# Kernel tuning notes

Measured on AMD Instinct MI355X. Metric: run time of the kernel, lower is better.

## Reference

```python
import math
import jax, jax.numpy as jnp
import numpy as np

D = 256       # d_model
R = 64        # low-rank bottleneck
E = 3         # num experts
KS = (1, 3, 5)
EPS = 0.1     # sinkhorn epsilon
ITERS = 10    # sinkhorn iterations


def _ln(x, g, b):
    m = jnp.mean(x, -1, keepdims=True)
    v = jnp.mean((x - m) ** 2, -1, keepdims=True)
    return (x - m) * jax.lax.rsqrt(v + 1e-5) * g + b


def _gelu(x):
    return jax.nn.gelu(x, approximate=False)  # torch nn.GELU default (erf)


def setup_inputs() -> dict:
    key = jax.random.key(0)
    ks = jax.random.split(key, 12)
    s = 0.02
    B, Lt, La = 16, 1024, 2048
    return {
        "text_feat": jax.random.normal(ks[0], (B, Lt, D), jnp.float32),
        "audio_feat": jax.random.normal(ks[1], (B, La, D), jnp.float32),
        # shared OT projection (LayerNorm + Linear, shared across modalities)
        "ln_g": jnp.ones((D,), jnp.float32),
        "ln_b": jnp.zeros((D,), jnp.float32),
        "W_sh": jax.random.normal(ks[2], (D, D), jnp.float32) * s,
        "b_sh": jnp.zeros((D,), jnp.float32),
        # contradiction router: Linear(d+1->d) GELU Linear(d->E)
        "Wr1": jax.random.normal(ks[3], (D, D + 1), jnp.float32) * s,
        "br1": jnp.zeros((D,), jnp.float32),
        "Wr2": jax.random.normal(ks[4], (E, D), jnp.float32) * s,
        "br2": jnp.zeros((E,), jnp.float32),
        # 3 low-rank conv experts (stacked where shapes match)
        "down_W": jax.random.normal(ks[5], (E, R, D), jnp.float32) * s,
        "down_b": jnp.zeros((E, R), jnp.float32),
        "conv_w1": jax.random.normal(ks[6], (R, R, 1), jnp.float32) * s,
        "conv_w3": jax.random.normal(ks[7], (R, R, 3), jnp.float32) * s,
        "conv_w5": jax.random.normal(ks[8], (R, R, 5), jnp.float32) * s,
        "conv_b": jnp.zeros((E, R), jnp.float32),
        "up_W": jax.random.normal(ks[9], (E, D, R), jnp.float32) * s,
        "up_b": jnp.zeros((E, D), jnp.float32),
        "en_g": jnp.ones((E, D), jnp.float32),
        "en_b": jnp.zeros((E, D), jnp.float32),
    }


def reference(text_feat, audio_feat, ln_g, ln_b, W_sh, b_sh, Wr1, br1, Wr2, br2,
              down_W, down_b, conv_w1, conv_w3, conv_w5, conv_b, up_W, up_b, en_g, en_b):
    B, Lt, _ = text_feat.shape
    La = audio_feat.shape[1]

    # ---- shared projection (dropout = identity at eval) ----
    Tp = _ln(text_feat, ln_g, ln_b) @ W_sh.T + b_sh      # [B,Lt,D]
    Ap = _ln(audio_feat, ln_g, ln_b) @ W_sh.T + b_sh     # [B,La,D]

    # ---- cosine cost ----
    Tn = Tp / jnp.maximum(jnp.linalg.norm(Tp, axis=-1, keepdims=True), 1e-12)
    An = Ap / jnp.maximum(jnp.linalg.norm(Ap, axis=-1, keepdims=True), 1e-12)
    cost = 1.0 - jnp.einsum('bmd,bnd->bmn', Tn, An)      # [B,Lt,La]

    # ---- log-domain Sinkhorn (uniform marginals, no masks) ----
    log_K = -cost / (EPS + 1e-8)
    log_mu = jnp.full((B, Lt), -math.log(Lt), jnp.float32)
    log_nu = jnp.full((B, La), -math.log(La), jnp.float32)
    lu = jnp.zeros((B, Lt), jnp.float32)
    lv = jnp.zeros((B, La), jnp.float32)
    for _ in range(ITERS):
        lu = log_mu - jax.scipy.special.logsumexp(log_K + lv[:, None, :], axis=-1)
        lu = jnp.nan_to_num(jnp.clip(lu, -1e9, 1e9), nan=0.0, posinf=1e9, neginf=-1e9)
        lv = log_nu - jax.scipy.special.logsumexp(log_K + lu[:, :, None], axis=1)
        lv = jnp.nan_to_num(jnp.clip(lv, -1e9, 1e9), nan=0.0, posinf=1e9, neginf=-1e9)
    pi = jnp.exp(lu[:, :, None] + log_K + lv[:, None, :])
    pi = jnp.nan_to_num(pi, nan=0.0, posinf=1.0, neginf=0.0)  # [B,Lt,La]

    A_al = jnp.einsum('bmn,bnd->bmd', pi, Ap)            # [B,Lt,D]
    S = jnp.sum(Tp * A_al, -1)                           # [B,Lt]
    resid = jnp.abs(Tp - A_al)                           # [B,Lt,D]

    # ---- contradiction router ----
    rin = jnp.concatenate([S[..., None], resid], -1)     # [B,Lt,D+1]
    G = jax.nn.softmax(_gelu(rin @ Wr1.T + br1) @ Wr2.T + br2, axis=-1)  # [B,Lt,E]

    # ---- multi-scale low-rank conv MoE over contradiction residual ----
    convs = (conv_w1, conv_w3, conv_w5)
    x = resid
    out = jnp.zeros_like(Tp)
    for e in range(E):
        h = _gelu(x @ down_W[e].T + down_b[e])           # [B,Lt,R]
        k = convs[e].shape[-1]
        pad = (k - 1) // 2
        hc = jax.lax.conv_general_dilated(
            h.transpose(0, 2, 1), convs[e], (1,), [(pad, pad)],
            dimension_numbers=('NCH', 'OIH', 'NCH')) + conv_b[e][None, :, None]
        h = _gelu(hc).transpose(0, 2, 1)                 # [B,Lt,R]
        h = h @ up_W[e].T + up_b[e]                      # [B,Lt,D]
        eo = _ln(h + x, en_g[e], en_b[e])
        out = out + G[..., e:e + 1] * eo
    return out
```

## Files before the change

### kernel.cpp

```cpp
#include <hip/hip_runtime.h>
#include <cstdio>

#define D_ 256
#define LT 1024
#define LA 2048
#define NB 16
#define RR_ 64
#define NRT (NB*LT)
#define NRA (NB*LA)

#define DECQ  (-0.080645161f)
#define DECQ2 (-0.11634637f)

typedef short bf16x8 __attribute__((ext_vector_type(8)));
typedef float f32x4 __attribute__((ext_vector_type(4)));

__device__ __forceinline__ float gelu_f(float x) {
    return 0.5f * x * (1.0f + erff(x * 0.70710678118654752f));
}
__device__ __forceinline__ unsigned short f2bf(float f) {
    union { float f; unsigned int i; } c; c.f = f;
    unsigned int x = c.i;
    return (unsigned short)((x + 0x7fffu + ((x >> 16) & 1u)) >> 16);
}
__device__ __forceinline__ float exp2_fast(float x) {
#if __has_builtin(__builtin_amdgcn_exp2f)
    return __builtin_amdgcn_exp2f(x);
#else
    float r; asm("v_exp_f32 %0, %1" : "=v"(r) : "v"(x)); return r;
#endif
}
__device__ __forceinline__ unsigned int cvt_pk_bf16(float lo, float hi) {
    unsigned int r;
    asm("v_cvt_pk_bf16_f32 %0, %1, %2" : "=v"(r) : "v"(lo), "v"(hi));
    return r;
}

__global__ __launch_bounds__(256) void k_prep_all(
    const float* __restrict__ W_sh, const float* __restrict__ down_W,
    const float* __restrict__ up_W, const float* __restrict__ Wr1,
    unsigned short* __restrict__ Wb, unsigned short* __restrict__ dWb,
    unsigned short* __restrict__ uWb, unsigned short* __restrict__ Wr1b)
{
    int i = blockIdx.x * 256 + threadIdx.x;
    if (i < 65536) Wb[i] = f2bf(W_sh[i]);
    else if (i < 114688) { int j = i - 65536; dWb[j] = f2bf(down_W[j]); }
    else if (i < 163840) { int j = i - 114688; uWb[j] = f2bf(up_W[j]); }
    else { int j = i - 163840; int n = j >> 8, k = j & 255; Wr1b[j] = f2bf(Wr1[(long)n * 257 + 1 + k]); }
}

__global__ __launch_bounds__(256) void k_lnproj_fused(
    const float* __restrict__ Xt, const float* __restrict__ Xa,
    const float* __restrict__ g, const float* __restrict__ bln,
    const unsigned short* __restrict__ Wb, const float* __restrict__ bsh,
    float* __restrict__ Tp, unsigned short* __restrict__ Tnb,
    unsigned short* __restrict__ Anb, unsigned short* __restrict__ ApbT)
{
    __shared__ short smem[64 * 264 + 256 * 40];
    short (*xb)[264] = (short(*)[264])smem;
    short (*Bs)[40]  = (short(*)[40])(smem + 64 * 264);
    short (*tt)[72]  = (short(*)[72])smem;
    int tid = threadIdx.x;
    int bid = blockIdx.x;
    bool is_text = bid < (NRT / 64);
    const float* X = is_text ? Xt : Xa;
    long row0 = is_text ? (long)bid * 64 : (long)(bid - NRT / 64) * 64;
    {
        int lane = tid & 31, rg = tid >> 5;
        float4 ga = *(const float4*)(g + lane * 8);
        float4 gb2 = *(const float4*)(g + lane * 8 + 4);
        float4 ba = *(const float4*)(bln + lane * 8);
        float4 bb2 = *(const float4*)(bln + lane * 8 + 4);
        for (int it = 0; it < 8; it++) {
            int r = it * 8 + rg;
            const float4* xp4 = (const float4*)(X + (row0 + r) * D_);
            float4 a = xp4[lane * 2], b = xp4[lane * 2 + 1];
            float s = a.x + a.y + a.z + a.w + b.x + b.y + b.z + b.w;
#pragma unroll
            for (int off = 16; off >= 1; off >>= 1) s += __shfl_xor(s, off);
            float mean = s * (1.0f / 256.0f);
            float q = (a.x - mean) * (a.x - mean) + (a.y - mean) * (a.y - mean)
                    + (a.z - mean) * (a.z - mean) + (a.w - mean) * (a.w - mean)
                    + (b.x - mean) * (b.x - mean) + (b.y - mean) * (b.y - mean)
                    + (b.z - mean) * (b.z - mean) + (b.w - mean) * (b.w - mean);
#pragma unroll
            for (int off = 16; off >= 1; off >>= 1) q += __shfl_xor(q, off);
            float ivar = rsqrtf(q * (1.0f / 256.0f) + 1e-5f);
            float v0 = (a.x - mean) * ivar * ga.x + ba.x;
            float v1 = (a.y - mean) * ivar * ga.y + ba.y;
            float v2 = (a.z - mean) * ivar * ga.z + ba.z;
            float v3 = (a.w - mean) * ivar * ga.w + ba.w;
            float v4 = (b.x - mean) * ivar * gb2.x + bb2.x;
            float v5 = (b.y - mean) * ivar * gb2.y + bb2.y;
            float v6 = (b.z - mean) * ivar * gb2.z + bb2.z;
            float v7 = (b.w - mean) * ivar * gb2.w + bb2.w;
            int4 pv;
            pv.x = (int)cvt_pk_bf16(v0, v1); pv.y = (int)cvt_pk_bf16(v2, v3);
            pv.z = (int)cvt_pk_bf16(v4, v5); pv.w = (int)cvt_pk_bf16(v6, v7);
            *(int4*)&xb[r][lane * 8] = pv;
        }
    }
    __syncthreads();
    int wid = tid >> 6, lane = tid & 63;
    int l15 = lane & 15, kq = lane >> 4;
    int m_local = wid * 16;
    f32x4 acc[16];
#pragma unroll
    for (int j = 0; j < 16; j++) acc[j] = (f32x4){0.f, 0.f, 0.f, 0.f};
    for (int kt = 0; kt < 8; kt++) {
        int k0 = kt * 32;
#pragma unroll
        for (int h = 0; h < 4; h++) {
            int idx = tid + 256 * h;
            int n = idx >> 2, qc = idx & 3;
            *(int4*)&Bs[n][qc * 8] = *(const int4*)(Wb + (long)n * D_ + k0 + qc * 8);
        }
        __syncthreads();
        bf16x8 af = *(const bf16x8*)&xb[m_local + l15][k0 + kq * 8];
#pragma unroll
        for (int j = 0; j < 16; j++) {
            bf16x8 bf = *(const bf16x8*)&Bs[j * 16 + l15][kq * 8];
            acc[j] = __builtin_amdgcn_mfma_f32_16x16x32_bf16(af, bf, acc[j], 0, 0, 0);
        }
        __syncthreads();
    }
#pragma unroll
    for (int j = 0; j < 16; j++) {
        float bv = bsh[j * 16 + l15];
#pragma unroll
        for (int r = 0; r < 4; r++) acc[j][r] += bv;
    }
    float sq[4] = {0.f, 0.f, 0.f, 0.f};
#pragma unroll
    for (int j = 0; j < 16; j++)
#pragma unroll
        for (int r = 0; r < 4; r++) sq[r] += acc[j][r] * acc[j][r];
#pragma unroll
    for (int off = 8; off >= 1; off >>= 1) {
#pragma unroll
        for (int r = 0; r < 4; r++) sq[r] += __shfl_xor(sq[r], off);
    }
    float rinv[4];
#pragma unroll
    for (int r = 0; r < 4; r++) rinv[r] = 1.0f / fmaxf(sqrtf(sq[r]), 1e-12f);
    if (is_text) {
#pragma unroll
        for (int j = 0; j < 16; j++) {
            int col = j * 16 + l15;
#pragma unroll
            for (int r = 0; r < 4; r++) {
                long m = row0 + m_local + kq * 4 + r;
                Tp[m * D_ + col] = acc[j][r];
                Tnb[m * D_ + col] = f2bf(acc[j][r] * rinv[r]);
            }
        }
    } else {
#pragma unroll
        for (int j = 0; j < 16; j++) {
            int col = j * 16 + l15;
#pragma unroll
            for (int r = 0; r < 4; r++) {
                int rloc = m_local + kq * 4 + r;
                unsigned short qv = f2bf(acc[j][r] * rinv[r]);
                Anb[(row0 + rloc) * D_ + col] = qv;
                tt[col][rloc] = (short)qv;
            }
        }
        __syncthreads();
        int b = (int)(row0 >> 11);
        int n0 = (int)(row0 & 2047);
#pragma unroll
        for (int h = 0; h < 8; h++) {
            int ci = tid + 256 * h;
            int col = ci >> 3, nch = ci & 7;
            int4 v = *(const int4*)&tt[col][nch * 8];
            *(int4*)(ApbT + ((long)b * D_ + col) * LA + n0 + nch * 8) = v;
        }
    }
}

__global__ __launch_bounds__(256) void k_cost_mfma(
    const unsigned short* __restrict__ Tnb, const unsigned short* __restrict__ Anb,
    unsigned char* __restrict__ logK8, unsigned char* __restrict__ logK8T)
{
    __shared__ short sm[2][128][48];
    short (*As)[48] = sm[0];
    short (*Bs)[48] = sm[1];
    unsigned char* tile = (unsigned char*)sm;
    int b = blockIdx.x;
    int m_blk = blockIdx.y * 128, n_blk = blockIdx.z * 128;
    int tid = threadIdx.x;
    int wid = tid >> 6, lane = tid & 63;
    int l15 = lane & 15, kq = lane >> 4;
    int wm0 = (wid >> 1) * 64, wn0 = (wid & 1) * 64;
    const unsigned short* Ab = Tnb + ((long)b * LT + m_blk) * D_;
    const unsigned short* Bb = Anb + ((long)b * LA + n_blk) * D_;
    f32x4 acc[4][4];
#pragma unroll
    for (int i = 0; i < 4; i++)
#pragma unroll
        for (int j = 0; j < 4; j++) acc[i][j] = (f32x4){0.f, 0.f, 0.f, 0.f};
    for (int kt = 0; kt < 8; kt++) {
        int k0 = kt * 32;
#pragma unroll
        for (int h = 0; h < 2; h++) {
            int idx = tid + 256 * h;
            int row = idx >> 2, ch = idx & 3;
            *(int4*)&As[row][ch * 8] = *(const int4*)(Ab + (long)row * D_ + k0 + ch * 8);
            *(int4*)&Bs[row][ch * 8] = *(const int4*)(Bb + (long)row * D_ + k0 + ch * 8);
        }
        __syncthreads();
        bf16x8 af[4], bfv[4];
#pragma unroll
        for (int i = 0; i < 4; i++) af[i] = *(const bf16x8*)&As[wm0 + i * 16 + l15][kq * 8];
#pragma unroll
        for (int j = 0; j < 4; j++) bfv[j] = *(const bf16x8*)&Bs[wn0 + j * 16 + l15][kq * 8];
#pragma unroll
        for (int i = 0; i < 4; i++)
#pragma unroll
            for (int j = 0; j < 4; j++)
                acc[i][j] = __builtin_amdgcn_mfma_f32_16x16x32_bf16(af[i], bfv[j], acc[i][j], 0, 0, 0);
        __syncthreads();
    }
#pragma unroll
    for (int i = 0; i < 4; i++) {
#pragma unroll
        for (int j = 0; j < 4; j++) {
            int n = wn0 + j * 16 + l15;
            long base = ((long)b * LT + m_blk + wm0 + i * 16 + kq * 4) * (long)LA + n_blk + n;
            unsigned int pk = 0;
#pragma unroll
            for (int r = 0; r < 4; r++) {
                float q = rintf((1.0f - acc[i][j][r]) * 124.0f);
                q = fminf(fmaxf(q, 0.0f), 255.0f);
                unsigned int qb = (unsigned int)q;
                pk |= qb << (8 * r);
                logK8[base + (long)r * LA] = (unsigned char)qb;
            }
            *(unsigned int*)&tile[n * 144 + wm0 + i * 16 + kq * 4] = pk;
        }
    }
    __syncthreads();
#pragma unroll
    for (int h = 0; h < 4; h++) {
        int idx = tid + 256 * h;
        int row = idx >> 3, ch = idx & 7;
        int4 v = *(const int4*)&tile[row * 144 + ch * 16];
        *(int4*)(logK8T + ((long)b * LA + n_blk + row) * (long)LT + m_blk + ch * 16) = v;
    }
}

__global__ __launch_bounds__(256) void k_rowlse3(
    const unsigned char* __restrict__ logK8, const float* __restrict__ lv2,
    float* __restrict__ lu2, int first)
{
    __shared__ float red[2][2];
    int b = blockIdx.x & 15;
    int mseg = blockIdx.x >> 4;
    int tid = threadIdx.x;
    int row = tid >> 7;
    int ln = tid & 127;
    float lvv[16];
    if (!first) {
        const float* lvp = lv2 + (long)b * LA + ln * 16;
#pragma unroll
        for (int k = 0; k < 4; k++) {
            float4 l = *(const float4*)(lvp + k * 4);
            lvv[k * 4 + 0] = l.x; lvv[k * 4 + 1] = l.y;
            lvv[k * 4 + 2] = l.z; lvv[k * 4 + 3] = l.w;
        }
    } else {
#pragma unroll
        for (int k = 0; k < 16; k++) lvv[k] = 0.f;
    }
    const unsigned char* p = logK8 + ((long)b * LT + mseg * 2 + row) * (long)LA + ln * 16;
    uint4 w = *(const uint4*)p;
    unsigned int ws4[4] = {w.x, w.y, w.z, w.w};
    float s = 0.f;
#pragma unroll
    for (int k = 0; k < 4; k++) {
        unsigned int u = ws4[k];
        s += exp2_fast(fmaf((float)(u & 0xffu),         DECQ2, lvv[k * 4 + 0]));
        s += exp2_fast(fmaf((float)((u >> 8) & 0xffu),  DECQ2, lvv[k * 4 + 1]));
        s += exp2_fast(fmaf((float)((u >> 16) & 0xffu), DECQ2, lvv[k * 4 + 2]));
        s += exp2_fast(fmaf((float)(u >> 24),           DECQ2, lvv[k * 4 + 3]));
    }
#pragma unroll
    for (int off = 32; off >= 1; off >>= 1) s += __shfl_xor(s, off);
    if ((tid & 63) == 0) red[row][(tid >> 6) & 1] = s;
    __syncthreads();
    if (tid < 2) {
        float sr = red[tid][0] + red[tid][1];
        lu2[(long)b * LT + mseg * 2 + tid] = -10.0f - __log2f(sr);
    }
}

__global__ __launch_bounds__(256) void k_collse3(
    const unsigned char* __restrict__ logK8T, const float* __restrict__ lu2,
    float* __restrict__ lv2)
{
    int b = blockIdx.x & 15;
    int nseg = blockIdx.x >> 4;
    int tid = threadIdx.x;
    int wv = tid >> 6, lane = tid & 63;
    int c = nseg * 4 + wv;
    float lus[16];
    const float* lup = lu2 + (long)b * LT + lane * 16;
#pragma unroll
    for (int k = 0; k < 4; k++) {
        float4 l = *(const float4*)(lup + k * 4);
        lus[k * 4 + 0] = l.x; lus[k * 4 + 1] = l.y;
        lus[k * 4 + 2] = l.z; lus[k * 4 + 3] = l.w;
    }
    const unsigned char* p = logK8T + ((long)b * LA + c) * (long)LT + lane * 16;
    uint4 w = *(const uint4*)p;
    unsigned int ws4[4] = {w.x, w.y, w.z, w.w};
    float s = 0.f;
#pragma unroll
    for (int k = 0; k < 4; k++) {
        unsigned int u = ws4[k];
        s += exp2_fast(fmaf((float)(u & 0xffu),         DECQ2, lus[k * 4 + 0]));
        s += exp2_fast(fmaf((float)((u >> 8) & 0xffu),  DECQ2, lus[k * 4 + 1]));
        s += exp2_fast(fmaf((float)((u >> 16) & 0xffu), DECQ2, lus[k * 4 + 2]));
        s += exp2_fast(fmaf((float)(u >> 24),           DECQ2, lus[k * 4 + 3]));
    }
#pragma unroll
    for (int off = 32; off >= 1; off >>= 1) s += __shfl_xor(s, off);
    if (lane == 0) lv2[(long)b * LA + c] = -11.0f - __log2f(s);
}

__global__ __launch_bounds__(256) void k_pi2(
    const unsigned char* __restrict__ logK8, const unsigned short* __restrict__ Ap,
    const float* __restrict__ lu2, const float* __restrict__ lv2,
    float* __restrict__ Apart)
{
    __shared__ short As[64][56];
    __shared__ short Bs[256][56];
    __shared__ float lv_s[1024];
    __shared__ float eus[64];
    int b = blockIdx.x;
    int kh = blockIdx.y;
    int m_blk = blockIdx.z * 64;
    int nbase = kh * 1024;
    int tid = threadIdx.x;
    for (int i = tid; i < 1024; i += 256) lv_s[i] = lv2[(long)b * LA + nbase + i];
    if (tid < 64) eus[tid] = exp2_fast(lu2[(long)b * LT + m_blk + tid]);
    __syncthreads();
    int wid = tid >> 6, lane = tid & 63;
    int l15 = lane & 15, kq = lane >> 4;
    int wm0 = (wid & 1) * 32, wd0 = (wid >> 1) * 128;
    f32x4 acc[2][8];
#pragma unroll
    for (int i = 0; i < 2; i++)
#pragma unroll
        for (int j = 0; j < 8; j++) acc[i][j] = (f32x4){0.f, 0.f, 0.f, 0.f};
    const unsigned char* Kbase = logK8 + ((long)b * LT + m_blk) * (long)LA + nbase;
    const unsigned short* Bbase = Ap + (long)b * D_ * (long)LA + nbase;
    int arow = tid >> 2, ac8 = (tid & 3) * 8;
    for (int kt = 0; kt < 32; kt++) {
        int n0 = kt * 32;
        {
            uint2 raw = *(const uint2*)(Kbase + (long)arow * LA + n0 + ac8);
            const float* lvp = &lv_s[n0 + ac8];
            unsigned int w0 = raw.x, w1 = raw.y;
            float e0 = exp2_fast(fmaf((float)(w0 & 0xffu),         DECQ2, lvp[0]));
            float e1 = exp2_fast(fmaf((float)((w0 >> 8) & 0xffu),  DECQ2, lvp[1]));
            float e2 = exp2_fast(fmaf((float)((w0 >> 16) & 0xffu), DECQ2, lvp[2]));
            float e3 = exp2_fast(fmaf((float)(w0 >> 24),           DECQ2, lvp[3]));
            float e4 = exp2_fast(fmaf((float)(w1 & 0xffu),         DECQ2, lvp[4]));
            float e5 = exp2_fast(fmaf((float)((w1 >> 8) & 0xffu),  DECQ2, lvp[5]));
            float e6 = exp2_fast(fmaf((float)((w1 >> 16) & 0xffu), DECQ2, lvp[6]));
            float e7 = exp2_fast(fmaf((float)(w1 >> 24),           DECQ2, lvp[7]));
            int4 ov;
            ov.x = (int)cvt_pk_bf16(e0, e1); ov.y = (int)cvt_pk_bf16(e2, e3);
            ov.z = (int)cvt_pk_bf16(e4, e5); ov.w = (int)cvt_pk_bf16(e6, e7);
            *(int4*)&As[arow][ac8] = ov;
        }
#pragma unroll
        for (int h = 0; h < 4; h++) {
            int idx = tid + 256 * h;
            int row = idx >> 2, ch = idx & 3;
            *(int4*)&Bs[row][ch * 8] = *(const int4*)(Bbase + (long)row * LA + n0 + ch * 8);
        }
        __syncthreads();
        bf16x8 af[2], bfv[8];
        af[0] = *(const bf16x8*)&As[wm0 + l15][kq * 8];
        af[1] = *(const bf16x8*)&As[wm0 + 16 + l15][kq * 8];
#pragma unroll
        for (int j = 0; j < 8; j++) bfv[j] = *(const bf16x8*)&Bs[wd0 + j * 16 + l15][kq * 8];
#pragma unroll
        for (int i = 0; i < 2; i++)
#pragma unroll
            for (int j = 0; j < 8; j++)
                acc[i][j] = __builtin_amdgcn_mfma_f32_16x16x32_bf16(af[i], bfv[j], acc[i][j], 0, 0, 0);
        __syncthreads();
    }
    float* dst = Apart + (long)kh * (NB * (long)LT * D_);
#pragma unroll
    for (int i = 0; i < 2; i++) {
#pragma unroll
        for (int r = 0; r < 4; r++) {
            int rloc = wm0 + i * 16 + kq * 4 + r;
            float eu = eus[rloc];
            int m = m_blk + rloc;
            long obase = ((long)b * LT + m) * D_;
#pragma unroll
            for (int j = 0; j < 8; j++)
                dst[obase + wd0 + j * 16 + l15] = acc[i][j][r] * eu;
        }
    }
}

__global__ __launch_bounds__(256) void k_sresid(
    const float* __restrict__ Tp, const float* __restrict__ Apart,
    float* __restrict__ resid, unsigned short* __restrict__ residb, float* __restrict__ S)
{
    __shared__ float red[4];
    int b = blockIdx.x & 15;
    int m = blockIdx.x >> 4;
    long row = (long)b * LT + m;
    int tid = threadIdx.x;
    long idx = row * D_ + tid;
    float t = Tp[idx];
    float a = Apart[idx] + Apart[idx + (long)NB * LT * D_];
    float rr = fabsf(t - a);
    resid[idx] = rr;
    residb[idx] = f2bf(rr);
    float p = t * a;
#pragma unroll
    for (int off = 32; off >= 1; off >>= 1) p += __shfl_xor(p, off);
    if ((tid & 63) == 0) red[tid >> 6] = p;
    __syncthreads();
    if (tid == 0) S[row] = red[0] + red[1] + red[2] + red[3];
}

__global__ __launch_bounds__(256) void k_router_fused(
    const unsigned short* __restrict__ residb, const unsigned short* __restrict__ Wr1b,
    const float* __restrict__ Wr1, const float* __restrict__ br1,
    const float* __restrict__ S, const float* __restrict__ Wr2,
    const float* __restrict__ br2, float* __restrict__ G)
{
    __shared__ short xb[16][264];
    __shared__ short Bs[256][40];
    __shared__ float red[4][3][16];
    int tid = threadIdx.x;
    long row0 = (long)blockIdx.x * 16;
#pragma unroll
    for (int h = 0; h < 2; h++) {
        int idx = tid + 256 * h;
        int row = idx >> 5, ch = idx & 31;
        *(int4*)&xb[row][ch * 8] = *(const int4*)(residb + (row0 + row) * D_ + ch * 8);
    }
    __syncthreads();
    int wid = tid >> 6, lane = tid & 63;
    int l15 = lane & 15, kq = lane >> 4;
    f32x4 acc[4];
#pragma unroll
    for (int j = 0; j < 4; j++) acc[j] = (f32x4){0.f, 0.f, 0.f, 0.f};
    for (int kt = 0; kt < 8; kt++) {
        int k0 = kt * 32;
#pragma unroll
        for (int h = 0; h < 4; h++) {
            int idx = tid + 256 * h;
            int n = idx >> 2, qc = idx & 3;
            *(int4*)&Bs[n][qc * 8] = *(const int4*)(Wr1b + (long)n * D_ + k0 + qc * 8);
        }
        __syncthreads();
        bf16x8 af = *(const bf16x8*)&xb[l15][k0 + kq * 8];
#pragma unroll
        for (int j = 0; j < 4; j++) {
            bf16x8 bf = *(const bf16x8*)&Bs[wid * 64 + j * 16 + l15][kq * 8];
            acc[j] = __builtin_amdgcn_mfma_f32_16x16x32_bf16(af, bf, acc[j], 0, 0, 0);
        }
        __syncthreads();
    }
    float sv[4];
#pragma unroll
    for (int r = 0; r < 4; r++) sv[r] = S[row0 + kq * 4 + r];
    float le[3][4] = {};
#pragma unroll
    for (int j = 0; j < 4; j++) {
        int col = wid * 64 + j * 16 + l15;
        float w0 = Wr1[(long)col * 257];
        float bv = br1[col];
        float w2a = Wr2[col], w2b = Wr2[256 + col], w2c = Wr2[512 + col];
#pragma unroll
        for (int r = 0; r < 4; r++) {
            float hv = gelu_f(acc[j][r] + sv[r] * w0 + bv);
            le[0][r] += hv * w2a;
            le[1][r] += hv * w2b;
            le[2][r] += hv * w2c;
        }
    }
#pragma unroll
    for (int off = 8; off >= 1; off >>= 1)
#pragma unroll
        for (int e = 0; e < 3; e++)
#pragma unroll
            for (int r = 0; r < 4; r++) le[e][r] += __shfl_xor(le[e][r], off);
    if (l15 == 0) {
#pragma unroll
        for (int e = 0; e < 3; e++)
#pragma unroll
            for (int r = 0; r < 4; r++) red[wid][e][kq * 4 + r] = le[e][r];
    }
    __syncthreads();
    if (tid < 16) {
        float L0 = red[0][0][tid] + red[1][0][tid] + red[2][0][tid] + red[3][0][tid] + br2[0];
        float L1 = red[0][1][tid] + red[1][1][tid] + red[2][1][tid] + red[3][1][tid] + br2[1];
        float L2 = red[0][2][tid] + red[1][2][tid] + red[2][2][tid] + red[3][2][tid] + br2[2];
        float mx = fmaxf(L0, fmaxf(L1, L2));
        float e0 = __expf(L0 - mx), e1 = __expf(L1 - mx), e2 = __expf(L2 - mx);
        float inv = 1.0f / (e0 + e1 + e2);
        long m = row0 + tid;
        G[m] = e0 * inv; G[NRT + m] = e1 * inv; G[2 * NRT + m] = e2 * inv;
    }
}

__global__ __launch_bounds__(256) void k_down_mfma(
    const unsigned short* __restrict__ residb, const unsigned short* __restrict__ dWb,
    const float* __restrict__ db, float* __restrict__ hall)
{
    __shared__ short xb[64][264];
    __shared__ short Bs[64][40];
    int tid = threadIdx.x;
    int e = blockIdx.y;
    int b = blockIdx.x & 15;
    int mseg = blockIdx.x >> 4;
    long row0 = (long)b * LT + mseg * 64;
    const unsigned short* dWe = dWb + (long)e * RR_ * D_;
    float* h = hall + (long)e * NRT * RR_;
#pragma unroll
    for (int hh = 0; hh < 8; hh++) {
        int idx = tid + 256 * hh;
        int row = idx >> 5, ch = idx & 31;
        *(int4*)&xb[row][ch * 8] = *(const int4*)(residb + (row0 + row) * D_ + ch * 8);
    }
    __syncthreads();
    int wid = tid >> 6, lane = tid & 63;
    int l15 = lane & 15, kq = lane >> 4;
    int m_local = wid * 16;
    f32x4 acc[4];
#pragma unroll
    for (int j = 0; j < 4; j++) acc[j] = (f32x4){0.f, 0.f, 0.f, 0.f};
    for (int kt = 0; kt < 8; kt++) {
        int k0 = kt * 32;
        {
            int n = tid >> 2, qc = tid & 3;
            *(int4*)&Bs[n][qc * 8] = *(const int4*)(dWe + (long)n * D_ + k0 + qc * 8);
        }
        __syncthreads();
        bf16x8 af = *(const bf16x8*)&xb[m_local + l15][k0 + kq * 8];
#pragma unroll
        for (int j = 0; j < 4; j++) {
            bf16x8 bf = *(const bf16x8*)&Bs[j * 16 + l15][kq * 8];
            acc[j] = __builtin_amdgcn_mfma_f32_16x16x32_bf16(af, bf, acc[j], 0, 0, 0);
        }
        __syncthreads();
    }
#pragma unroll
    for (int j = 0; j < 4; j++) {
        int col = j * 16 + l15;
        float bv = db[e * RR_ + col];
#pragma unroll
        for (int r = 0; r < 4; r++) {
            long m = row0 + m_local + kq * 4 + r;
            h[m * RR_ + col] = gelu_f(acc[j][r] + bv);
        }
    }
}

__global__ __launch_bounds__(256) void k_conv_all(
    const float* __restrict__ hall, const float* __restrict__ cw1,
    const float* __restrict__ cw3, const float* __restrict__ cw5,
    const float* __restrict__ conv_b, unsigned short* __restrict__ hcbb)
{
    __shared__ float hs[68][68];
    __shared__ float wt[64][64];
    int e = blockIdx.y;
    const float* w = (e == 0) ? cw1 : ((e == 1) ? cw3 : cw5);
    int ksz = (e == 0) ? 1 : ((e == 1) ? 3 : 5);
    const float* h = hall + (long)e * NRT * RR_;
    unsigned short* hcb = hcbb + (long)e * NRT * RR_;
    const float* cb = conv_b + e * 64;
    int b = blockIdx.x & 15;
    int m0 = (blockIdx.x >> 4) * 64;
    int tid = threadIdx.x;
    int pad = (ksz - 1) >> 1;
    for (int idx = tid; idx < 68 * 16; idx += 256) {
        int mr = idx >> 4, i4 = idx & 15;
        int mm = m0 - 2 + mr;
        float4 vv = { 0.f, 0.f, 0.f, 0.f };
        if (mm >= 0 && mm < LT) vv = *(const float4*)(h + ((long)b * LT + mm) * RR_ + i4 * 4);
        *(float4*)&hs[mr][i4 * 4] = vv;
    }
    int tx = tid & 15, ty = tid >> 4;
    float acc[4][4] = {};
    for (int t = 0; t < ksz; t++) {
        __syncthreads();
        for (int idx = tid; idx < 4096; idx += 256) {
            int i = idx & 63, j = idx >> 6;
            wt[i][j] = w[(long)j * RR_ * ksz + i * ksz + t];
        }
        __syncthreads();
        int roff = ty * 4 + 2 + t - pad;
        for (int i4 = 0; i4 < 16; i4++) {
            float4 h0 = *(const float4*)&hs[roff + 0][i4 * 4];
            float4 h1 = *(const float4*)&hs[roff + 1][i4 * 4];
            float4 h2 = *(const float4*)&hs[roff + 2][i4 * 4];
            float4 h3 = *(const float4*)&hs[roff + 3][i4 * 4];
            float hh[4][4] = { { h0.x, h0.y, h0.z, h0.w }, { h1.x, h1.y, h1.z, h1.w },
                               { h2.x, h2.y, h2.z, h2.w }, { h3.x, h3.y, h3.z, h3.w } };
#pragma unroll
            for (int s = 0; s < 4; s++) {
                float4 wv = *(const float4*)&wt[i4 * 4 + s][tx * 4];
#pragma unroll
                for (int r = 0; r < 4; r++) {
                    acc[r][0] += hh[r][s] * wv.x;
                    acc[r][1] += hh[r][s] * wv.y;
                    acc[r][2] += hh[r][s] * wv.z;
                    acc[r][3] += hh[r][s] * wv.w;
                }
            }
        }
    }
    float4 bb = *(const float4*)(cb + tx * 4);
#pragma unroll
    for (int r = 0; r < 4; r++) {
        long m = (long)b * LT + m0 + ty * 4 + r;
        unsigned long long pv =
              (unsigned long long)cvt_pk_bf16(gelu_f(acc[r][0] + bb.x), gelu_f(acc[r][1] + bb.y))
            | ((unsigned long long)cvt_pk_bf16(gelu_f(acc[r][2] + bb.z), gelu_f(acc[r][3] + bb.w)) << 32);
        *(unsigned long long*)(hcb + m * RR_ + tx * 4) = pv;
    }
}

__global__ __launch_bounds__(256) void k_up3(
    const unsigned short* __restrict__ hcbb, const unsigned short* __restrict__ uWb,
    const float* __restrict__ up_b, const float* __restrict__ resid,
    const float* __restrict__ en_g, const float* __restrict__ en_b,
    const float* __restrict__ G, float* __restrict__ out)
{
    __shared__ short hs[64][88];
    __shared__ short Bs[256][40];
    int tid = threadIdx.x;
    int b = blockIdx.x & 15;
    int mseg = blockIdx.x >> 4;
    long row0 = (long)b * LT + mseg * 64;
    int wid = tid >> 6, lane = tid & 63;
    int l15 = lane & 15, kq = lane >> 4;
    int m_local = wid * 16;
    long mrow[4];
#pragma unroll
    for (int r = 0; r < 4; r++) mrow[r] = row0 + m_local + kq * 4 + r;
    f32x4 outacc[16];
#pragma unroll
    for (int j = 0; j < 16; j++) outacc[j] = (f32x4){0.f, 0.f, 0.f, 0.f};
    for (int e = 0; e < 3; e++) {
        __syncthreads();
        const unsigned short* hcb = hcbb + (long)e * NRT * RR_;
        const unsigned short* uWe = uWb + (long)e * 16384;
#pragma unroll
        for (int hh = 0; hh < 2; hh++) {
            int idx = tid + 256 * hh;
            int row = idx >> 3, ch = idx & 7;
            *(int4*)&hs[row][ch * 8] = *(const int4*)(hcb + (row0 + row) * RR_ + ch * 8);
        }
        f32x4 acc[16];
#pragma unroll
        for (int j = 0; j < 16; j++) acc[j] = (f32x4){0.f, 0.f, 0.f, 0.f};
        for (int kt = 0; kt < 2; kt++) {
            int k0 = kt * 32;
#pragma unroll
            for (int hh = 0; hh < 4; hh++) {
                int idx = tid + 256 * hh;
                int n = idx >> 2, qc = idx & 3;
                *(int4*)&Bs[n][qc * 8] = *(const int4*)(uWe + (long)n * RR_ + k0 + qc * 8);
            }
            __syncthreads();
            bf16x8 af = *(const bf16x8*)&hs[m_local + l15][k0 + kq * 8];
#pragma unroll
            for (int j = 0; j < 16; j++) {
                bf16x8 bf = *(const bf16x8*)&Bs[j * 16 + l15][kq * 8];
                acc[j] = __builtin_amdgcn_mfma_f32_16x16x32_bf16(af, bf, acc[j], 0, 0, 0);
            }
            __syncthreads();
        }
        const float* ub = up_b + e * 256;
#pragma unroll
        for (int j = 0; j < 16; j++) {
            int col = j * 16 + l15;
            float bv = ub[col];
#pragma unroll
            for (int r = 0; r < 4; r++)
                acc[j][r] += bv + resid[mrow[r] * D_ + col];
        }
        float s[4] = {0.f, 0.f, 0.f, 0.f};
#pragma unroll
        for (int j = 0; j < 16; j++)
#pragma unroll
            for (int r = 0; r < 4; r++) s[r] += acc[j][r];
#pragma unroll
        for (int off = 8; off >= 1; off >>= 1)
#pragma unroll
            for (int r = 0; r < 4; r++) s[r] += __shfl_xor(s[r], off);
        float mn[4];
#pragma unroll
        for (int r = 0; r < 4; r++) mn[r] = s[r] * (1.0f / 256.0f);
        float q[4] = {0.f, 0.f, 0.f, 0.f};
#pragma unroll
        for (int j = 0; j < 16; j++)
#pragma unroll
            for (int r = 0; r < 4; r++) { float d = acc[j][r] - mn[r]; q[r] += d * d; }
#pragma unroll
        for (int off = 8; off >= 1; off >>= 1)
#pragma unroll
            for (int r = 0; r < 4; r++) q[r] += __shfl_xor(q[r], off);
        float iv[4], gv[4];
#pragma unroll
        for (int r = 0; r < 4; r++) {
            iv[r] = rsqrtf(q[r] * (1.0f / 256.0f) + 1e-5f);
            gv[r] = G[(long)e * NRT + mrow[r]];
        }
        const float* eg = en_g + e * 256;
        const float* eb = en_b + e * 256;
#pragma unroll
        for (int j = 0; j < 16; j++) {
            int col = j * 16 + l15;
            float egc = eg[col], ebc = eb[col];
#pragma unroll
            for (int r = 0; r < 4; r++)
                outacc[j][r] += gv[r] * ((acc[j][r] - mn[r]) * iv[r] * egc + ebc);
        }
    }
#pragma unroll
    for (int j = 0; j < 16; j++) {
        int col = j * 16 + l15;
#pragma unroll
        for (int r = 0; r < 4; r++)
            out[mrow[r] * D_ + col] = outacc[j][r];
    }
}

extern "C" void kernel_launch(void* const* d_in, const int* in_sizes, int n_in,
                              void* d_out, int out_size, void* d_ws, size_t ws_size,
                              hipStream_t stream)
{
    const float* text   = (const float*)d_in[0];
    const float* audio  = (const float*)d_in[1];
    const float* ln_g   = (const float*)d_in[2];
    const float* ln_b   = (const float*)d_in[3];
    const float* W_sh   = (const float*)d_in[4];
    const float* b_sh   = (const float*)d_in[5];
    const float* Wr1    = (const float*)d_in[6];
    const float* br1    = (const float*)d_in[7];
    const float* Wr2    = (const float*)d_in[8];
    const float* br2    = (const float*)d_in[9];
    const float* down_W = (const float*)d_in[10];
    const float* down_b = (const float*)d_in[11];
    const float* cw1    = (const float*)d_in[12];
    const float* cw3    = (const float*)d_in[13];
    const float* cw5    = (const float*)d_in[14];
    const float* conv_b = (const float*)d_in[15];
    const float* up_W   = (const float*)d_in[16];
    const float* up_b   = (const float*)d_in[17];
    const float* en_g   = (const float*)d_in[18];
    const float* en_b   = (const float*)d_in[19];

    float* ws = (float*)d_ws;
    float*          Tp    = ws;
    unsigned short* Tnb   = (unsigned short*)(ws + 4194304);
    unsigned short* Anb   = (unsigned short*)(ws + 6291456);
    unsigned short* ApbT  = (unsigned short*)(ws + 10485760);
    unsigned char*  logK8 = (unsigned char*)(ws + 14680064);
    float*          Apart = ws + 23068672;
    float*          resid = ws + 31457280;
    unsigned short* residb= (unsigned short*)(ws + 35651584);
    float*          lu2   = ws + 37748736;
    float*          lv2   = ws + 37765120;
    float*          Sb    = ws + 37797888;
    float*          Gb    = ws + 37814272;
    unsigned short* Wb    = (unsigned short*)(ws + 37863424);
    unsigned short* dWb   = (unsigned short*)(ws + 37896192);
    unsigned short* uWb   = (unsigned short*)(ws + 37920768);
    unsigned short* Wr1b  = (unsigned short*)(ws + 37945344);
    size_t need_bytes = (size_t)37978112 * 4;
    if (ws_size < need_bytes) {
        fprintf(stderr, "kernel_launch: ws_size %zu < needed %zu\n", ws_size, need_bytes);
        return;
    }
    float*          hall = ws + 14680064;
    unsigned short* hcbb = (unsigned short*)(ws + 17825792);
    unsigned char*  logK8T = (unsigned char*)(ws + 23068672);

    k_prep_all<<<896, 256, 0, stream>>>(W_sh, down_W, up_W, Wr1, Wb, dWb, uWb, Wr1b);
    k_lnproj_fused<<<(NRT + NRA) / 64, 256, 0, stream>>>(text, audio, ln_g, ln_b, Wb, b_sh,
                                                         Tp, Tnb, Anb, ApbT);
    k_cost_mfma<<<dim3(NB, LT / 128, LA / 128), 256, 0, stream>>>(Tnb, Anb, logK8, logK8T);
    for (int it = 0; it < 10; it++) {
        k_rowlse3<<<NRT / 2, 256, 0, stream>>>(logK8, lv2, lu2, it == 0 ? 1 : 0);
        k_collse3<<<NB * (LA / 4), 256, 0, stream>>>(logK8T, lu2, lv2);
    }
    k_pi2<<<dim3(NB, 2, LT / 64), 256, 0, stream>>>(logK8, ApbT, lu2, lv2, Apart);
    k_sresid<<<NRT, 256, 0, stream>>>(Tp, Apart, resid, residb, Sb);
    k_router_fused<<<NRT / 16, 256, 0, stream>>>(residb, Wr1b, Wr1, br1, Sb, Wr2, br2, Gb);
    k_down_mfma<<<dim3(NRT / 64, 3), 256, 0, stream>>>(residb, dWb, down_b, hall);
    k_conv_all<<<dim3(NRT / 64, 3), 256, 0, stream>>>(hall, cw1, cw3, cw5, conv_b, hcbb);
    k_up3<<<NRT / 64, 256, 0, stream>>>(hcbb, uWb, up_b, resid, en_g, en_b, Gb, (float*)d_out);
}
```

Measured before the change: 532.1 us.

## Read projection weights directly, batch Sinkhorn rows per block, store Apart as bf16

The LN+projection kernel now reads the bf16 weight fragments straight from global memory (L2-resident) instead of staging them in LDS, which removes the per-k-step LDS copy and two barriers. The Sinkhorn row and column log-sum-exp kernels each process four rows or columns per thread group, so one launch needs a quarter as many blocks. The partial aligned-audio output from k_pi2 is stored as bf16 rather than fp32, halving that intermediate's write and read traffic. This costs some precision in A_al and in the residual computed from it.

```diff
diff --git a/kernel.cpp b/kernel.cpp
--- a/kernel.cpp
+++ b/kernel.cpp
@@ -23,6 +23,9 @@
     unsigned int x = c.i;
     return (unsigned short)((x + 0x7fffu + ((x >> 16) & 1u)) >> 16);
 }
+__device__ __forceinline__ float bf2f(unsigned short u) {
+    return __uint_as_float((unsigned int)u << 16);
+}
 __device__ __forceinline__ float exp2_fast(float x) {
 #if __has_builtin(__builtin_amdgcn_exp2f)
     return __builtin_amdgcn_exp2f(x);
@@ -56,9 +59,8 @@
     float* __restrict__ Tp, unsigned short* __restrict__ Tnb,
     unsigned short* __restrict__ Anb, unsigned short* __restrict__ ApbT)
 {
-    __shared__ short smem[64 * 264 + 256 * 40];
+    __shared__ short smem[256 * 72];
     short (*xb)[264] = (short(*)[264])smem;
-    short (*Bs)[40]  = (short(*)[40])(smem + 64 * 264);
     short (*tt)[72]  = (short(*)[72])smem;
     int tid = threadIdx.x;
     int bid = blockIdx.x;
@@ -107,22 +109,15 @@
     f32x4 acc[16];
 #pragma unroll
     for (int j = 0; j < 16; j++) acc[j] = (f32x4){0.f, 0.f, 0.f, 0.f};
+    const unsigned short* Wfrag = Wb + (long)l15 * D_ + kq * 8;
     for (int kt = 0; kt < 8; kt++) {
         int k0 = kt * 32;
-#pragma unroll
-        for (int h = 0; h < 4; h++) {
-            int idx = tid + 256 * h;
-            int n = idx >> 2, qc = idx & 3;
-            *(int4*)&Bs[n][qc * 8] = *(const int4*)(Wb + (long)n * D_ + k0 + qc * 8);
-        }
-        __syncthreads();
         bf16x8 af = *(const bf16x8*)&xb[m_local + l15][k0 + kq * 8];
 #pragma unroll
         for (int j = 0; j < 16; j++) {
-            bf16x8 bf = *(const bf16x8*)&Bs[j * 16 + l15][kq * 8];
+            bf16x8 bf = *(const bf16x8*)(Wfrag + (long)j * 16 * D_ + k0);
             acc[j] = __builtin_amdgcn_mfma_f32_16x16x32_bf16(af, bf, acc[j], 0, 0, 0);
         }
-        __syncthreads();
     }
 #pragma unroll
     for (int j = 0; j < 16; j++) {
@@ -155,6 +150,7 @@
             }
         }
     } else {
+        __syncthreads();
 #pragma unroll
         for (int j = 0; j < 16; j++) {
             int col = j * 16 + l15;
@@ -250,15 +246,15 @@
     }
 }
 
-__global__ __launch_bounds__(256) void k_rowlse3(
+__global__ __launch_bounds__(256) void k_rowlse4(
     const unsigned char* __restrict__ logK8, const float* __restrict__ lv2,
     float* __restrict__ lu2, int first)
 {
-    __shared__ float red[2][2];
+    __shared__ float red[8][2];
     int b = blockIdx.x & 15;
     int mseg = blockIdx.x >> 4;
     int tid = threadIdx.x;
-    int row = tid >> 7;
+    int rg = tid >> 7;
     int ln = tid & 127;
     float lvv[16];
     if (!first) {
@@ -273,29 +269,32 @@
 #pragma unroll
         for (int k = 0; k < 16; k++) lvv[k] = 0.f;
     }
-    const unsigned char* p = logK8 + ((long)b * LT + mseg * 2 + row) * (long)LA + ln * 16;
-    uint4 w = *(const uint4*)p;
-    unsigned int ws4[4] = {w.x, w.y, w.z, w.w};
-    float s = 0.f;
-#pragma unroll
-    for (int k = 0; k < 4; k++) {
-        unsigned int u = ws4[k];
-        s += exp2_fast(fmaf((float)(u & 0xffu),         DECQ2, lvv[k * 4 + 0]));
-        s += exp2_fast(fmaf((float)((u >> 8) & 0xffu),  DECQ2, lvv[k * 4 + 1]));
-        s += exp2_fast(fmaf((float)((u >> 16) & 0xffu), DECQ2, lvv[k * 4 + 2]));
-        s += exp2_fast(fmaf((float)(u >> 24),           DECQ2, lvv[k * 4 + 3]));
-    }
-#pragma unroll
-    for (int off = 32; off >= 1; off >>= 1) s += __shfl_xor(s, off);
-    if ((tid & 63) == 0) red[row][(tid >> 6) & 1] = s;
+    const unsigned char* p = logK8 + ((long)b * LT + mseg * 8 + rg * 4) * (long)LA + ln * 16;
+#pragma unroll
+    for (int r = 0; r < 4; r++) {
+        uint4 w = *(const uint4*)(p + (long)r * LA);
+        unsigned int ws4[4] = {w.x, w.y, w.z, w.w};
+        float s = 0.f;
+#pragma unroll
+        for (int k = 0; k < 4; k++) {
+            unsigned int u = ws4[k];
+            s += exp2_fast(fmaf((float)(u & 0xffu),         DECQ2, lvv[k * 4 + 0]));
+            s += exp2_fast(fmaf((float)((u >> 8) & 0xffu),  DECQ2, lvv[k * 4 + 1]));
+            s += exp2_fast(fmaf((float)((u >> 16) & 0xffu), DECQ2, lvv[k * 4 + 2]));
+            s += exp2_fast(fmaf((float)(u >> 24),           DECQ2, lvv[k * 4 + 3]));
+        }
+#pragma unroll
+        for (int off = 32; off >= 1; off >>= 1) s += __shfl_xor(s, off);
+        if ((tid & 63) == 0) red[rg * 4 + r][(tid >> 6) & 1] = s;
+    }
     __syncthreads();
-    if (tid < 2) {
+    if (tid < 8) {
         float sr = red[tid][0] + red[tid][1];
-        lu2[(long)b * LT + mseg * 2 + tid] = -10.0f - __log2f(sr);
-    }
-}
-
-__global__ __launch_bounds__(256) void k_collse3(
+        lu2[(long)b * LT + mseg * 8 + tid] = -10.0f - __log2f(sr);
+    }
+}
+
+__global__ __launch_bounds__(256) void k_collse4(
     const unsigned char* __restrict__ logK8T, const float* __restrict__ lu2,
     float* __restrict__ lv2)
 {
@@ -303,7 +302,6 @@
     int nseg = blockIdx.x >> 4;
     int tid = threadIdx.x;
     int wv = tid >> 6, lane = tid & 63;
-    int c = nseg * 4 + wv;
     float lus[16];
     const float* lup = lu2 + (long)b * LT + lane * 16;
 #pragma unroll
@@ -312,27 +310,31 @@
         lus[k * 4 + 0] = l.x; lus[k * 4 + 1] = l.y;
         lus[k * 4 + 2] = l.z; lus[k * 4 + 3] = l.w;
     }
-    const unsigned char* p = logK8T + ((long)b * LA + c) * (long)LT + lane * 16;
-    uint4 w = *(const uint4*)p;
-    unsigned int ws4[4] = {w.x, w.y, w.z, w.w};
-    float s = 0.f;
-#pragma unroll
-    for (int k = 0; k < 4; k++) {
-        unsigned int u = ws4[k];
-        s += exp2_fast(fmaf((float)(u & 0xffu),         DECQ2, lus[k * 4 + 0]));
-        s += exp2_fast(fmaf((float)((u >> 8) & 0xffu),  DECQ2, lus[k * 4 + 1]));
-        s += exp2_fast(fmaf((float)((u >> 16) & 0xffu), DECQ2, lus[k * 4 + 2]));
-        s += exp2_fast(fmaf((float)(u >> 24),           DECQ2, lus[k * 4 + 3]));
-    }
-#pragma unroll
-    for (int off = 32; off >= 1; off >>= 1) s += __shfl_xor(s, off);
-    if (lane == 0) lv2[(long)b * LA + c] = -11.0f - __log2f(s);
+    const unsigned char* p = logK8T + ((long)b * LA + nseg * 16 + wv * 4) * (long)LT + lane * 16;
+#pragma unroll
+    for (int cs = 0; cs < 4; cs++) {
+        uint4 w = *(const uint4*)(p + (long)cs * LT);
+        unsigned int ws4[4] = {w.x, w.y, w.z, w.w};
+        float s = 0.f;
+#pragma unroll
+        for (int k = 0; k < 4; k++) {
+            unsigned int u = ws4[k];
+            s += exp2_fast(fmaf((float)(u & 0xffu),         DECQ2, lus[k * 4 + 0]));
+            s += exp2_fast(fmaf((float)((u >> 8) & 0xffu),  DECQ2, lus[k * 4 + 1]));
+            s += exp2_fast(fmaf((float)((u >> 16) & 0xffu), DECQ2, lus[k * 4 + 2]));
+            s += exp2_fast(fmaf((float)(u >> 24),           DECQ2, lus[k * 4 + 3]));
+        }
+#pragma unroll
+        for (int off = 32; off >= 1; off >>= 1) s += __shfl_xor(s, off);
+        if (lane == 0)
+            lv2[(long)b * LA + nseg * 16 + wv * 4 + cs] = -11.0f - __log2f(s);
+    }
 }
 
 __global__ __launch_bounds__(256) void k_pi2(
     const unsigned char* __restrict__ logK8, const unsigned short* __restrict__ Ap,
     const float* __restrict__ lu2, const float* __restrict__ lv2,
-    float* __restrict__ Apart)
+    unsigned short* __restrict__ Apart)
 {
     __shared__ short As[64][56];
     __shared__ short Bs[256][56];
@@ -395,7 +397,7 @@
                 acc[i][j] = __builtin_amdgcn_mfma_f32_16x16x32_bf16(af[i], bfv[j], acc[i][j], 0, 0, 0);
         __syncthreads();
     }
-    float* dst = Apart + (long)kh * (NB * (long)LT * D_);
+    unsigned short* dst = Apart + (long)kh * (NB * (long)LT * D_);
 #pragma unroll
     for (int i = 0; i < 2; i++) {
 #pragma unroll
@@ -406,13 +408,13 @@
             long obase = ((long)b * LT + m) * D_;
 #pragma unroll
             for (int j = 0; j < 8; j++)
-                dst[obase + wd0 + j * 16 + l15] = acc[i][j][r] * eu;
+                dst[obase + wd0 + j * 16 + l15] = f2bf(acc[i][j][r] * eu);
         }
     }
 }
 
 __global__ __launch_bounds__(256) void k_sresid(
-    const float* __restrict__ Tp, const float* __restrict__ Apart,
+    const float* __restrict__ Tp, const unsigned short* __restrict__ Apart,
     float* __restrict__ resid, unsigned short* __restrict__ residb, float* __restrict__ S)
 {
     __shared__ float red[4];
@@ -422,7 +424,7 @@
     int tid = threadIdx.x;
     long idx = row * D_ + tid;
     float t = Tp[idx];
-    float a = Apart[idx] + Apart[idx + (long)NB * LT * D_];
+    float a = bf2f(Apart[idx]) + bf2f(Apart[idx + (long)NB * LT * D_]);
     float rr = fabsf(t - a);
     resid[idx] = rr;
     residb[idx] = f2bf(rr);
@@ -773,7 +775,7 @@
     unsigned short* Anb   = (unsigned short*)(ws + 6291456);
     unsigned short* ApbT  = (unsigned short*)(ws + 10485760);
     unsigned char*  logK8 = (unsigned char*)(ws + 14680064);
-    float*          Apart = ws + 23068672;
+    unsigned short* Apart = (unsigned short*)(ws + 23068672);
     float*          resid = ws + 31457280;
     unsigned short* residb= (unsigned short*)(ws + 35651584);
     float*          lu2   = ws + 37748736;
@@ -798,8 +800,8 @@
                                                          Tp, Tnb, Anb, ApbT);
     k_cost_mfma<<<dim3(NB, LT / 128, LA / 128), 256, 0, stream>>>(Tnb, Anb, logK8, logK8T);
     for (int it = 0; it < 10; it++) {
-        k_rowlse3<<<NRT / 2, 256, 0, stream>>>(logK8, lv2, lu2, it == 0 ? 1 : 0);
-        k_collse3<<<NB * (LA / 4), 256, 0, stream>>>(logK8T, lu2, lv2);
+        k_rowlse4<<<NRT / 8, 256, 0, stream>>>(logK8, lv2, lu2, it == 0 ? 1 : 0);
+        k_collse4<<<NB * (LA / 16), 256, 0, stream>>>(logK8T, lu2, lv2);
     }
     k_pi2<<<dim3(NB, 2, LT / 64), 256, 0, stream>>>(logK8, ApbT, lu2, lv2, Apart);
     k_sresid<<<NRT, 256, 0, stream>>>(Tp, Apart, resid, residb, Sb);
```

New measurement: 542.0 us. Within noise of the previous version (+1.9%).
